# Performance work log

Hardware: AMD Instinct MI355X
Metric: run time of the kernel (lower is better)

Reference implementation:

```python
import jax, jax.numpy as jnp
import numpy as np

N_PTS = 2097152
RES = 512
C_FEAT = 32
MAT_IDS = ((0, 1), (0, 2), (1, 2))


def grid_sample_plane(plane, gx, gy):
    """Bilinear grid_sample, align_corners=False, zero padding.
    plane: [C, H, W]; gx, gy: [N] normalized coords in [-1, 1]
    (gx indexes width / last axis, gy indexes height, matching torch).
    Returns [C, N]."""
    C, H, W = plane.shape
    # align_corners=False unnormalization
    ix = ((gx + 1.0) * W - 1.0) * 0.5
    iy = ((gy + 1.0) * H - 1.0) * 0.5
    x0 = jnp.floor(ix)
    y0 = jnp.floor(iy)
    x1 = x0 + 1.0
    y1 = y0 + 1.0
    wx1 = ix - x0
    wx0 = 1.0 - wx1
    wy1 = iy - y0
    wy0 = 1.0 - wy1

    def corner(xi, yi, w):
        valid = (xi >= 0) & (xi <= W - 1) & (yi >= 0) & (yi <= H - 1)
        xc = jnp.clip(xi, 0, W - 1).astype(jnp.int32)
        yc = jnp.clip(yi, 0, H - 1).astype(jnp.int32)
        vals = plane[:, yc, xc]  # [C, N] gather
        return vals * (w * valid.astype(w.dtype))[None, :]

    return (corner(x0, y0, wx0 * wy0) + corner(x1, y0, wx1 * wy0)
            + corner(x0, y1, wx0 * wy1) + corner(x1, y1, wx1 * wy1))


def setup_inputs() -> dict:
    key = jax.random.key(0)
    kx, kc = jax.random.split(key)
    x = jax.random.uniform(kx, (N_PTS, 3), dtype=jnp.float32, minval=-1.0, maxval=1.0)
    C_mat = jax.random.normal(kc, (3, C_FEAT, RES, RES), dtype=jnp.float32)
    return {"x": x, "C_mat": C_mat}


def reference(x, C_mat):
    # bound = 1 -> x / bound is a no-op
    feat = None
    for p in range(3):
        i, j = MAT_IDS[p]
        f = grid_sample_plane(C_mat[p], x[:, i], x[:, j])  # [C, N]
        feat = f if feat is None else feat + f
    return feat.T  # [N, C]
```

## Files before the change

### kernel.cpp

```cpp
#include <hip/hip_runtime.h>
#include <hip/hip_fp16.h>

#define RES 512
#define CF 32
#define PLANE_ELEMS (RES * RES)

__global__ __launch_bounds__(256) void triplane_transpose(
    const float* __restrict__ C_mat, __half* __restrict__ ws) {
    int gid = blockIdx.x * 256 + threadIdx.x;
    int x  = gid & (RES - 1);
    int py = gid >> 9;
    int p  = py >> 9;
    int y  = py & (RES - 1);
    const float* src = C_mat + (size_t)p * CF * PLANE_ELEMS + (size_t)y * RES + x;

    __half tmp[CF];
#pragma unroll
    for (int c = 0; c < CF; ++c) {
        tmp[c] = __float2half(src[(size_t)c * PLANE_ELEMS]);
    }
    float4* dst = (float4*)(ws + (size_t)gid * CF);
    const float4* t4 = (const float4*)tmp;
#pragma unroll
    for (int k = 0; k < 4; ++k) dst[k] = t4[k];
}

__global__ __launch_bounds__(256) void triplane_sample(
    const float* __restrict__ xin, const __half* __restrict__ planes,
    float* __restrict__ out, int n_pts) {
    int gid = blockIdx.x * 256 + threadIdx.x;
    int n   = gid >> 2;
    int sub = gid & 3;
    if (n >= n_pts) return;

    float c0 = xin[3 * n + 0];
    float c1 = xin[3 * n + 1];
    float c2 = xin[3 * n + 2];
    float coord[3] = {c0, c1, c2};
    const int ii[3] = {0, 0, 1};
    const int jj[3] = {1, 2, 2};

    float acc[8];
#pragma unroll
    for (int k = 0; k < 8; ++k) acc[k] = 0.0f;

#pragma unroll
    for (int p = 0; p < 3; ++p) {
        float gx = coord[ii[p]];
        float gy = coord[jj[p]];
        float ix = ((gx + 1.0f) * (float)RES - 1.0f) * 0.5f;
        float iy = ((gy + 1.0f) * (float)RES - 1.0f) * 0.5f;
        float x0f = floorf(ix), y0f = floorf(iy);
        float wx1 = ix - x0f,  wy1 = iy - y0f;
        float wx0 = 1.0f - wx1, wy0 = 1.0f - wy1;
        int x0 = (int)x0f, y0 = (int)y0f;
        int x1 = x0 + 1,   y1 = y0 + 1;

        const __half* pbase = planes + (size_t)p * PLANE_ELEMS * CF + (size_t)sub * 8;

        int   cxs[4] = {x0, x1, x0, x1};
        int   cys[4] = {y0, y0, y1, y1};
        float cws[4] = {wx0 * wy0, wx1 * wy0, wx0 * wy1, wx1 * wy1};
#pragma unroll
        for (int c = 0; c < 4; ++c) {
            int xi = cxs[c], yi = cys[c];
            bool valid = (xi >= 0) & (xi <= RES - 1) & (yi >= 0) & (yi <= RES - 1);
            int xc = min(max(xi, 0), RES - 1);
            int yc = min(max(yi, 0), RES - 1);
            float w = valid ? cws[c] : 0.0f;
            float4 raw = *(const float4*)(pbase + ((size_t)yc * RES + xc) * CF);
            const __half2* h2 = (const __half2*)&raw;
#pragma unroll
            for (int k = 0; k < 4; ++k) {
                float2 f = __half22float2(h2[k]);
                acc[2 * k + 0] += w * f.x;
                acc[2 * k + 1] += w * f.y;
            }
        }
    }

    float4* o = (float4*)(out + (size_t)n * CF + (size_t)sub * 8);
    o[0] = make_float4(acc[0], acc[1], acc[2], acc[3]);
    o[1] = make_float4(acc[4], acc[5], acc[6], acc[7]);
}

__global__ __launch_bounds__(256) void triplane_sample_direct(
    const float* __restrict__ xin, const float* __restrict__ C_mat,
    float* __restrict__ out, int n_pts) {
    int gid = blockIdx.x * 256 + threadIdx.x;
    int n   = gid >> 2;
    int sub = gid & 3;
    if (n >= n_pts) return;

    float coord[3] = {xin[3 * n], xin[3 * n + 1], xin[3 * n + 2]};
    const int ii[3] = {0, 0, 1};
    const int jj[3] = {1, 2, 2};

    float acc[8];
#pragma unroll
    for (int k = 0; k < 8; ++k) acc[k] = 0.0f;

    for (int p = 0; p < 3; ++p) {
        float gx = coord[ii[p]];
        float gy = coord[jj[p]];
        float ix = ((gx + 1.0f) * (float)RES - 1.0f) * 0.5f;
        float iy = ((gy + 1.0f) * (float)RES - 1.0f) * 0.5f;
        float x0f = floorf(ix), y0f = floorf(iy);
        float wx1 = ix - x0f,  wy1 = iy - y0f;
        float wx0 = 1.0f - wx1, wy0 = 1.0f - wy1;
        int x0 = (int)x0f, y0 = (int)y0f;
        int x1 = x0 + 1,   y1 = y0 + 1;

        int   cxs[4] = {x0, x1, x0, x1};
        int   cys[4] = {y0, y0, y1, y1};
        float cws[4] = {wx0 * wy0, wx1 * wy0, wx0 * wy1, wx1 * wy1};
        for (int c = 0; c < 4; ++c) {
            int xi = cxs[c], yi = cys[c];
            bool valid = (xi >= 0) & (xi <= RES - 1) & (yi >= 0) & (yi <= RES - 1);
            int xc = min(max(xi, 0), RES - 1);
            int yc = min(max(yi, 0), RES - 1);
            float w = valid ? cws[c] : 0.0f;
            size_t texel = (size_t)yc * RES + xc;
#pragma unroll
            for (int k = 0; k < 8; ++k) {
                float v = C_mat[((size_t)p * CF + sub * 8 + k) * PLANE_ELEMS + texel];
                acc[k] += w * v;
            }
        }
    }

    float4* o = (float4*)(out + (size_t)n * CF + (size_t)sub * 8);
    o[0] = make_float4(acc[0], acc[1], acc[2], acc[3]);
    o[1] = make_float4(acc[4], acc[5], acc[6], acc[7]);
}

extern "C" void kernel_launch(void* const* d_in, const int* in_sizes, int n_in,
                              void* d_out, int out_size, void* d_ws, size_t ws_size,
                              hipStream_t stream) {
    const float* x     = (const float*)d_in[0];
    const float* C_mat = (const float*)d_in[1];
    float* out = (float*)d_out;
    int n_pts = in_sizes[0] / 3;

    size_t need = (size_t)3 * PLANE_ELEMS * CF * sizeof(__half);
    int sample_blocks = (n_pts * 4 + 255) / 256;

    if (ws_size >= need) {
        __half* planes = (__half*)d_ws;
        int tblocks = (3 * PLANE_ELEMS) / 256;
        triplane_transpose<<<tblocks, 256, 0, stream>>>(C_mat, planes);
        triplane_sample<<<sample_blocks, 256, 0, stream>>>(x, planes, out, n_pts);
    } else {
        triplane_sample_direct<<<sample_blocks, 256, 0, stream>>>(x, C_mat, out, n_pts);
    }
}
```

Before: 655.8 us.

## Tile transpose through LDS and batch all gathers with nontemporal IO in sampler

Measured after the change: 664.2 us. Within noise of the previous version (+1.3%).

```diff
diff --git a/kernel.cpp b/kernel.cpp
--- a/kernel.cpp
+++ b/kernel.cpp
@@ -4,28 +4,50 @@
 #define RES 512
 #define CF 32
 #define PLANE_ELEMS (RES * RES)
+#define TX 128
+
+typedef float fvec4 __attribute__((ext_vector_type(4)));
 
 __global__ __launch_bounds__(256) void triplane_transpose(
     const float* __restrict__ C_mat, __half* __restrict__ ws) {
-    int gid = blockIdx.x * 256 + threadIdx.x;
-    int x  = gid & (RES - 1);
-    int py = gid >> 9;
-    int p  = py >> 9;
-    int y  = py & (RES - 1);
-    const float* src = C_mat + (size_t)p * CF * PLANE_ELEMS + (size_t)y * RES + x;
+    __shared__ float tile[CF][TX + 1];
 
-    __half tmp[CF];
+    int b  = blockIdx.x;
+    int xc = b & 3;
+    int y  = (b >> 2) & (RES - 1);
+    int p  = b >> 11;
+    int x0 = xc * TX;
+    int t  = threadIdx.x;
+
+    int c = t >> 3;
+    int j = t & 7;
+    const float* src = C_mat + (((size_t)(p * CF + c)) << 18) + (size_t)y * RES + x0 + j * 4;
 #pragma unroll
-    for (int c = 0; c < CF; ++c) {
-        tmp[c] = __float2half(src[(size_t)c * PLANE_ELEMS]);
+    for (int k = 0; k < 4; ++k) {
+        fvec4 v = *(const fvec4*)(src + k * 32);
+        int xl = j * 4 + k * 32;
+        tile[c][xl + 0] = v.x;
+        tile[c][xl + 1] = v.y;
+        tile[c][xl + 2] = v.z;
+        tile[c][xl + 3] = v.w;
     }
-    float4* dst = (float4*)(ws + (size_t)gid * CF);
-    const float4* t4 = (const float4*)tmp;
+    __syncthreads();
+
+    int xr = t >> 1;
+    int h  = t & 1;
+    __half hv[16] __attribute__((aligned(16)));
 #pragma unroll
-    for (int k = 0; k < 4; ++k) dst[k] = t4[k];
+    for (int q = 0; q < 16; ++q) {
+        hv[q] = __float2half(tile[h * 16 + q][xr]);
+    }
+    size_t rec = ((size_t)(p * RES + y) * RES + x0 + xr);
+    fvec4* dst = (fvec4*)(ws + rec * CF + h * 16);
+    const fvec4* s4 = (const fvec4*)hv;
+    dst[0] = s4[0];
+    dst[1] = s4[1];
 }
 
-__global__ __launch_bounds__(256) void triplane_sample(
+__global__ __launch_bounds__(256, 4) void triplane_sample(
     const float* __restrict__ xin, const __half* __restrict__ planes,
     float* __restrict__ out, int n_pts) {
     int gid = blockIdx.x * 256 + threadIdx.x;
@@ -33,55 +55,68 @@
     int sub = gid & 3;
     if (n >= n_pts) return;
 
-    float c0 = xin[3 * n + 0];
-    float c1 = xin[3 * n + 1];
-    float c2 = xin[3 * n + 2];
-    float coord[3] = {c0, c1, c2};
-    const int ii[3] = {0, 0, 1};
-    const int jj[3] = {1, 2, 2};
+    float cx = __builtin_nontemporal_load(xin + 3 * n + 0);
+    float cy = __builtin_nontemporal_load(xin + 3 * n + 1);
+    float cz = __builtin_nontemporal_load(xin + 3 * n + 2);
+    float gxs[3] = {cx, cx, cy};
+    float gys[3] = {cy, cz, cz};
+
+    int   offs[12];
+    float wgt[12];
+
+#pragma unroll
+    for (int p = 0; p < 3; ++p) {
+        float ix = ((gxs[p] + 1.0f) * (float)RES - 1.0f) * 0.5f;
+        float iy = ((gys[p] + 1.0f) * (float)RES - 1.0f) * 0.5f;
+        float x0f = floorf(ix), y0f = floorf(iy);
+        float wx1 = ix - x0f,  wy1 = iy - y0f;
+        float wx0 = 1.0f - wx1, wy0 = 1.0f - wy1;
+        int x0 = (int)x0f, y0 = (int)y0f;
+        int x1 = x0 + 1,   y1 = y0 + 1;
+
+        int   cxs[4] = {x0, x1, x0, x1};
+        int   cys[4] = {y0, y0, y1, y1};
+        float cws[4] = {wx0 * wy0, wx1 * wy0, wx0 * wy1, wx1 * wy1};
+        int pbase = p * (PLANE_ELEMS * CF * 2);
+#pragma unroll
+        for (int cc = 0; cc < 4; ++cc) {
+            int xi = cxs[cc], yi = cys[cc];
+            bool valid = ((unsigned)xi < (unsigned)RES) & ((unsigned)yi < (unsigned)RES);
+            int xcl = min(max(xi, 0), RES - 1);
+            int ycl = min(max(yi, 0), RES - 1);
+            wgt[p * 4 + cc]  = valid ? cws[cc] : 0.0f;
+            offs[p * 4 + cc] = pbase + ((ycl << 9) + xcl) * (CF * 2);
+        }
+    }
+
+    const char* pb = (const char*)planes + sub * 16;
+    fvec4 raw[12];
+#pragma unroll
+    for (int l = 0; l < 12; ++l) {
+        raw[l] = *(const fvec4*)(pb + offs[l]);
+    }
 
     float acc[8];
 #pragma unroll
     for (int k = 0; k < 8; ++k) acc[k] = 0.0f;
 
 #pragma unroll
-    for (int p = 0; p < 3; ++p) {
-        float gx = coord[ii[p]];
-        float gy = coord[jj[p]];
-        float ix = ((gx + 1.0f) * (float)RES - 1.0f) * 0.5f;
-        float iy = ((gy + 1.0f) * (float)RES - 1.0f) * 0.5f;
-        float x0f = floorf(ix), y0f = floorf(iy);
-        float wx1 = ix - x0f,  wy1 = iy - y0f;
-        float wx0 = 1.0f - wx1, wy0 = 1.0f - wy1;
-        int x0 = (int)x0f, y0 = (int)y0f;
-        int x1 = x0 + 1,   y1 = y0 + 1;
-
-        const __half* pbase = planes + (size_t)p * PLANE_ELEMS * CF + (size_t)sub * 8;
-
-        int   cxs[4] = {x0, x1, x0, x1};
-        int   cys[4] = {y0, y0, y1, y1};
-        float cws[4] = {wx0 * wy0, wx1 * wy0, wx0 * wy1, wx1 * wy1};
+    for (int l = 0; l < 12; ++l) {
+        const __half2* h2 = (const __half2*)&raw[l];
+        float w = wgt[l];
 #pragma unroll
-        for (int c = 0; c < 4; ++c) {
-            int xi = cxs[c], yi = cys[c];
-            bool valid = (xi >= 0) & (xi <= RES - 1) & (yi >= 0) & (yi <= RES - 1);
-            int xc = min(max(xi, 0), RES - 1);
-            int yc = min(max(yi, 0), RES - 1);
-            float w = valid ? cws[c] : 0.0f;
-            float4 raw = *(const float4*)(pbase + ((size_t)yc * RES + xc) * CF);
-            const __half2* h2 = (const __half2*)&raw;
-#pragma unroll
-            for (int k = 0; k < 4; ++k) {
-                float2 f = __half22float2(h2[k]);
-                acc[2 * k + 0] += w * f.x;
-                acc[2 * k + 1] += w * f.y;
-            }
+        for (int k = 0; k < 4; ++k) {
+            float2 f = __half22float2(h2[k]);
+            acc[2 * k + 0] += w * f.x;
+            acc[2 * k + 1] += w * f.y;
         }
     }
 
-    float4* o = (float4*)(out + (size_t)n * CF + (size_t)sub * 8);
-    o[0] = make_float4(acc[0], acc[1], acc[2], acc[3]);
-    o[1] = make_float4(acc[4], acc[5], acc[6], acc[7]);
+    float* o = out + (size_t)n * CF + (size_t)sub * 8;
+    fvec4 o0 = {acc[0], acc[1], acc[2], acc[3]};
+    fvec4 o1 = {acc[4], acc[5], acc[6], acc[7]};
+    __builtin_nontemporal_store(o0, (fvec4*)o);
+    __builtin_nontemporal_store(o1, (fvec4*)(o + 4));
 }
 
 __global__ __launch_bounds__(256) void triplane_sample_direct(
@@ -147,7 +182,7 @@
 
     if (ws_size >= need) {
         __half* planes = (__half*)d_ws;
-        int tblocks = (3 * PLANE_ELEMS) / 256;
+        int tblocks = 3 * RES * (RES / TX);
         triplane_transpose<<<tblocks, 256, 0, stream>>>(C_mat, planes);
         triplane_sample<<<sample_blocks, 256, 0, stream>>>(x, planes, out, n_pts);
     } else {
```
